# Kernel tuning notes

Hardware: AMD Instinct MI355X
Metric: run time of the kernel (lower is better)

The kernel has to match this reference:

```python
import jax, jax.numpy as jnp
import numpy as np

D = 1024
H = 16
HD = D // H  # 64


def setup_inputs() -> dict:
    key = jax.random.key(0)
    ks = jax.random.split(key, 12)
    B, S = 2, 2048
    inp = {
        "input_query": jax.random.normal(ks[0], (B, S, D), jnp.float32),
        "input_key": jax.random.normal(ks[1], (B, S, D), jnp.float32),
        "input_value": jax.random.normal(ks[2], (B, S, D), jnp.float32),
        "mask": jnp.ones((S, S), dtype=bool),  # ignored, as in original
        # per-head Q/K/V linears, stacked over heads: [H, D, HD]
        "Wq": jax.random.normal(ks[3], (H, D, HD), jnp.float32) / np.sqrt(D),
        "bq": jax.random.normal(ks[4], (H, HD), jnp.float32) * 0.01,
        "Wk": jax.random.normal(ks[5], (H, D, HD), jnp.float32) / np.sqrt(D),
        "bk": jax.random.normal(ks[6], (H, HD), jnp.float32) * 0.01,
        "Wv": jax.random.normal(ks[7], (H, D, HD), jnp.float32) / np.sqrt(D),
        "bv": jax.random.normal(ks[8], (H, HD), jnp.float32) * 0.01,
        "Wo": jax.random.normal(ks[9], (D, D), jnp.float32) / np.sqrt(D),
        "bo": jax.random.normal(ks[10], (D,), jnp.float32) * 0.01,
    }
    return inp


def reference(input_query, input_key, input_value, mask, Wq, bq, Wk, bk, Wv, bv, Wo, bo):
    B, S, _ = input_query.shape
    # batched per-head projections: [B,S,D] x [H,D,HD] -> [B,H,S,HD]
    q = jnp.einsum("bsd,hdk->bhsk", input_query, Wq) + bq[None, :, None, :]
    k = jnp.einsum("bsd,hdk->bhsk", input_key, Wk) + bk[None, :, None, :]
    v = jnp.einsum("bsd,hdk->bhsk", input_value, Wv) + bv[None, :, None, :]
    scale = 1.0 / np.sqrt(HD)
    scores = jnp.einsum("bhqk,bhsk->bhqs", q, k) * scale  # [B,H,S,S]
    causal = jnp.tril(jnp.ones((S, S), dtype=bool))
    scores = jnp.where(causal[None, None], scores, jnp.finfo(scores.dtype).min)
    p = jax.nn.softmax(scores, axis=-1)
    out = jnp.einsum("bhqs,bhsk->bhqk", p, v)  # [B,H,S,HD]
    # concat heads (matches torch.cat over head outputs on last dim)
    out = out.transpose(0, 2, 1, 3).reshape(B, S, D)
    return out @ Wo + bo
```

## Files before the change

kernel.cpp:

```cpp
#include <hip/hip_runtime.h>
#include <hip/hip_bf16.h>

typedef __bf16 bf16;
typedef bf16 bf16x8 __attribute__((ext_vector_type(8)));
typedef bf16 bf16x4 __attribute__((ext_vector_type(4)));
typedef float f32x4 __attribute__((ext_vector_type(4)));

#define B_  2
#define S_  2048
#define D_  1024
#define H_  16
#define HD_ 64
#define M_  4096
#define K_  1024
#define N_  1024

#if __has_builtin(__builtin_amdgcn_exp2f)
#define EXP2F(x) __builtin_amdgcn_exp2f(x)
#else
#define EXP2F(x) exp2f(x)
#endif

__device__ __forceinline__ void gld16(const bf16* g, bf16* l) {
    __builtin_amdgcn_global_load_lds(
        (const __attribute__((address_space(1))) unsigned int*)(g),
        (__attribute__((address_space(3))) unsigned int*)(l), 16, 0, 0);
}
__device__ __forceinline__ void gld16f(const float* g, float* l) {
    __builtin_amdgcn_global_load_lds(
        (const __attribute__((address_space(1))) unsigned int*)(g),
        (__attribute__((address_space(3))) unsigned int*)(l), 16, 0, 0);
}

__global__ void pack_w(const float* __restrict__ wq, const float* __restrict__ wk,
                       const float* __restrict__ wv, const float* __restrict__ wo,
                       bf16* __restrict__ out) {
    int t = blockIdx.y;
    bf16* dst = out + (size_t)t * N_ * K_;
    int o = blockIdx.x * 256 + threadIdx.x;
    int n = o >> 10, k = o & 1023;
    if (t == 3) {
        dst[o] = (bf16)wo[k * D_ + n];
    } else {
        const float* src = (t == 0) ? wq : (t == 1) ? wk : wv;
        dst[o] = (bf16)src[(n >> 6) * (D_ * HD_) + k * HD_ + (n & 63)];
    }
}

__global__ __launch_bounds__(256) void gemm_qkv(
        const float* __restrict__ xq, const float* __restrict__ xk,
        const float* __restrict__ xv, const bf16* __restrict__ Wt,
        const float* __restrict__ bq, const float* __restrict__ bk,
        const float* __restrict__ bv, bf16* __restrict__ QKV) {
    __shared__ __align__(16) float Af[2][128 * 32];
    __shared__ __align__(16) bf16 Bs[2][128 * 32];
    int t = blockIdx.z;
    const float* A = (t == 0) ? xq : (t == 1) ? xk : xv;
    const bf16* W = Wt + (size_t)t * N_ * K_;
    const float* bias = (t == 0) ? bq : (t == 1) ? bk : bv;
    int m0 = blockIdx.x * 128, n0 = blockIdx.y * 128;
    int tid = threadIdx.x;
    int w = tid >> 6, l = tid & 63, lr = l & 15, lg = l >> 4;
    int wr = (w >> 1) * 64, wc = (w & 1) * 64;
    int srow = (l >> 2), scol = (l & 3) * 8;
    size_t aoff[4];
    #pragma unroll
    for (int c = 0; c < 4; c++) {
        int chunk = w * 256 + c * 64 + l;
        int r = chunk >> 3, p = chunk & 7;
        aoff[c] = (size_t)(m0 + r) * K_ + ((p ^ (r & 7)) << 2);
    }
    f32x4 acc[4][4] = {};
    #pragma unroll
    for (int c = 0; c < 4; c++)
        gld16f(A + aoff[c], &Af[0][(w * 256 + c * 64) * 4]);
    #pragma unroll
    for (int c = 0; c < 2; c++) {
        int chunk = w * 2 + c;
        gld16(&W[(size_t)(n0 + chunk * 16 + srow) * K_ + scol], &Bs[0][chunk * 512]);
    }
    __syncthreads();
    for (int k0 = 0; k0 < K_; k0 += 32) {
        int cur = (k0 >> 5) & 1, nxt = cur ^ 1;
        if (k0 + 32 < K_) {
            #pragma unroll
            for (int c = 0; c < 4; c++)
                gld16f(A + aoff[c] + k0 + 32, &Af[nxt][(w * 256 + c * 64) * 4]);
            #pragma unroll
            for (int c = 0; c < 2; c++) {
                int chunk = w * 2 + c;
                gld16(&W[(size_t)(n0 + chunk * 16 + srow) * K_ + k0 + 32 + scol], &Bs[nxt][chunk * 512]);
            }
        }
        bf16x8 af[4], bfr[4];
        #pragma unroll
        for (int mi = 0; mi < 4; mi++) {
            int r = wr + mi * 16 + lr;
            f32x4 a0 = *(const f32x4*)((const char*)Af[cur] + r * 128 + (((lg * 2) ^ (r & 7)) * 16));
            f32x4 a1 = *(const f32x4*)((const char*)Af[cur] + r * 128 + (((lg * 2 + 1) ^ (r & 7)) * 16));
            bf16x8 v = { (bf16)a0[0], (bf16)a0[1], (bf16)a0[2], (bf16)a0[3],
                         (bf16)a1[0], (bf16)a1[1], (bf16)a1[2], (bf16)a1[3] };
            af[mi] = v;
        }
        #pragma unroll
        for (int ni = 0; ni < 4; ni++) bfr[ni] = *(const bf16x8*)&Bs[cur][(wc + ni * 16 + lr) * 32 + lg * 8];
        #pragma unroll
        for (int mi = 0; mi < 4; mi++)
            #pragma unroll
            for (int ni = 0; ni < 4; ni++)
                acc[mi][ni] = __builtin_amdgcn_mfma_f32_16x16x32_bf16(af[mi], bfr[ni], acc[mi][ni], 0, 0, 0);
        __syncthreads();
    }
    float qscale = (t == 0) ? 0.125f * 1.4426950408889634f : 1.0f;
    #pragma unroll
    for (int mi = 0; mi < 4; mi++)
        #pragma unroll
        for (int ni = 0; ni < 4; ni++)
            #pragma unroll
            for (int i = 0; i < 4; i++) {
                int m = m0 + wr + mi * 16 + lg * 4 + i;
                int n = n0 + wc + ni * 16 + lr;
                float v = (acc[mi][ni][i] + bias[n]) * qscale;
                int b = m >> 11, s = m & 2047, h = n >> 6, hd = n & 63;
                QKV[((((size_t)t * B_ + b) * H_ + h) * S_ + s) * HD_ + hd] = (bf16)v;
            }
}

__global__ __launch_bounds__(256) void gemm_out(
        const bf16* __restrict__ A, const bf16* __restrict__ Wt,
        const float* __restrict__ bo, float* __restrict__ out) {
    __shared__ __align__(16) bf16 As[2][128 * 32];
    __shared__ __align__(16) bf16 Bs[2][128 * 32];
    int m0 = blockIdx.x * 128, n0 = blockIdx.y * 128;
    int tid = threadIdx.x;
    int w = tid >> 6, l = tid & 63, lr = l & 15, lg = l >> 4;
    int wr = (w >> 1) * 64, wc = (w & 1) * 64;
    int srow = (l >> 2), scol = (l & 3) * 8;
    f32x4 acc[4][4] = {};
    #pragma unroll
    for (int c = 0; c < 2; c++) {
        int chunk = w * 2 + c;
        gld16(&A[(size_t)(m0 + chunk * 16 + srow) * K_ + scol], &As[0][chunk * 512]);
        gld16(&Wt[(size_t)(n0 + chunk * 16 + srow) * K_ + scol], &Bs[0][chunk * 512]);
    }
    __syncthreads();
    for (int k0 = 0; k0 < K_; k0 += 32) {
        int cur = (k0 >> 5) & 1, nxt = cur ^ 1;
        if (k0 + 32 < K_) {
            #pragma unroll
            for (int c = 0; c < 2; c++) {
                int chunk = w * 2 + c;
                gld16(&A[(size_t)(m0 + chunk * 16 + srow) * K_ + k0 + 32 + scol], &As[nxt][chunk * 512]);
                gld16(&Wt[(size_t)(n0 + chunk * 16 + srow) * K_ + k0 + 32 + scol], &Bs[nxt][chunk * 512]);
            }
        }
        bf16x8 af[4], bfr[4];
        #pragma unroll
        for (int mi = 0; mi < 4; mi++) af[mi] = *(const bf16x8*)&As[cur][(wr + mi * 16 + lr) * 32 + lg * 8];
        #pragma unroll
        for (int ni = 0; ni < 4; ni++) bfr[ni] = *(const bf16x8*)&Bs[cur][(wc + ni * 16 + lr) * 32 + lg * 8];
        #pragma unroll
        for (int mi = 0; mi < 4; mi++)
            #pragma unroll
            for (int ni = 0; ni < 4; ni++)
                acc[mi][ni] = __builtin_amdgcn_mfma_f32_16x16x32_bf16(af[mi], bfr[ni], acc[mi][ni], 0, 0, 0);
        __syncthreads();
    }
    #pragma unroll
    for (int mi = 0; mi < 4; mi++)
        #pragma unroll
        for (int ni = 0; ni < 4; ni++)
            #pragma unroll
            for (int i = 0; i < 4; i++) {
                int m = m0 + wr + mi * 16 + lg * 4 + i;
                int n = n0 + wc + ni * 16 + lr;
                out[(size_t)m * N_ + n] = acc[mi][ni][i] + bo[n];
            }
}

__global__ __launch_bounds__(256) void transpose_v(const bf16* __restrict__ V,
                                                   bf16* __restrict__ VT) {
    __shared__ __align__(16) bf16 Ls[64][64];
    int s0 = blockIdx.x * 64, bh = blockIdx.y;
    const bf16* src = V + (size_t)bh * S_ * HD_;
    bf16* dst = VT + (size_t)bh * HD_ * S_;
    int tid = threadIdx.x;
    #pragma unroll
    for (int c = tid; c < 512; c += 256) {
        int row = c >> 3, cg = (c & 7) * 8;
        int cgp = cg ^ (((row >> 3) & 3) << 4);
        *(bf16x8*)&Ls[row][cgp] = *(const bf16x8*)&src[(size_t)(s0 + row) * 64 + cg];
    }
    __syncthreads();
    #pragma unroll
    for (int c = tid; c < 512; c += 256) {
        int hd = c >> 3, sg = (c & 7) * 8;
        bf16x8 v;
        #pragma unroll
        for (int e = 0; e < 8; e++) {
            int row = sg + e;
            v[e] = Ls[row][hd ^ (((row >> 3) & 3) << 4)];
        }
        *(bf16x8*)&dst[(size_t)hd * S_ + s0 + sg] = v;
    }
}

__global__ __launch_bounds__(512) void attn(const bf16* __restrict__ QKV,
                                            const bf16* __restrict__ VT,
                                            bf16* __restrict__ AO) {
    __shared__ __align__(16) bf16 Ks[2][64][72];
    __shared__ __align__(16) bf16 Vts[2][64][72];
    __shared__ __align__(16) bf16 Ps[8][16][72];
    int bh = blockIdx.y;
    int qt = (bh & 16) ? blockIdx.x : (15 - blockIdx.x);
    int q0 = qt * 128;
    const bf16* Qp = QKV + (size_t)bh * S_ * HD_;
    const bf16* Kp = QKV + (size_t)(32 + bh) * S_ * HD_;
    const bf16* VTp = VT + (size_t)bh * HD_ * S_;
    int tid = threadIdx.x, w = tid >> 6, l = tid & 63, lr = l & 15, lg = l >> 4;
    int srow = tid >> 3, scg = (tid & 7) * 8;

    bf16x8 aq[2];
    #pragma unroll
    for (int ks = 0; ks < 2; ks++)
        aq[ks] = *(const bf16x8*)&Qp[(size_t)(q0 + w * 16 + lr) * 64 + ks * 32 + lg * 8];

    f32x4 o[4] = {};
    float lsum[4] = {};
    int jmax = 2 * qt + 1;

    *(bf16x8*)&Ks[0][srow][scg]  = *(const bf16x8*)&Kp[(size_t)srow * 64 + scg];
    *(bf16x8*)&Vts[0][srow][scg] = *(const bf16x8*)&VTp[(size_t)srow * S_ + scg];
    __syncthreads();

    for (int j = 0; j <= jmax; ++j) {
        int cur = j & 1;
        bool pf = (j < jmax);
        bf16x8 kreg, vreg;
        if (pf) {
            kreg = *(const bf16x8*)&Kp[(size_t)((j + 1) * 64 + srow) * 64 + scg];
            vreg = *(const bf16x8*)&VTp[(size_t)srow * S_ + (j + 1) * 64 + scg];
        }

        f32x4 sc[4] = {};
        __builtin_amdgcn_s_setprio(1);
        #pragma unroll
        for (int ks = 0; ks < 2; ks++)
            #pragma unroll
            for (int ni = 0; ni < 4; ni++) {
                bf16x8 bk_ = *(const bf16x8*)&Ks[cur][ni * 16 + lr][ks * 32 + lg * 8];
                sc[ni] = __builtin_amdgcn_mfma_f32_16x16x32_bf16(aq[ks], bk_, sc[ni], 0, 0, 0);
            }
        __builtin_amdgcn_s_setprio(0);

        int qrow = w * 16 + lg * 4;
        int kvb = j * 64 - q0;
        if (j >= 2 * qt) {
            #pragma unroll
            for (int ni = 0; ni < 4; ni++)
                #pragma unroll
                for (int i = 0; i < 4; i++) {
                    float s = sc[ni][i];
                    if (kvb + ni * 16 + lr > qrow + i) s = -30000.0f;
                    float p = EXP2F(s);
                    lsum[i] += p;
                    Ps[w][lg * 4 + i][ni * 16 + lr] = (bf16)p;
                }
        } else {
            #pragma unroll
            for (int ni = 0; ni < 4; ni++)
                #pragma unroll
                for (int i = 0; i < 4; i++) {
                    float p = EXP2F(sc[ni][i]);
                    lsum[i] += p;
                    Ps[w][lg * 4 + i][ni * 16 + lr] = (bf16)p;
                }
        }

        __builtin_amdgcn_s_setprio(1);
        #pragma unroll
        for (int ks = 0; ks < 2; ks++) {
            bf16x8 ap = *(const bf16x8*)&Ps[w][lr][ks * 32 + lg * 8];
            #pragma unroll
            for (int nf = 0; nf < 4; nf++) {
                bf16x8 bv_ = *(const bf16x8*)&Vts[cur][nf * 16 + lr][ks * 32 + lg * 8];
                o[nf] = __builtin_amdgcn_mfma_f32_16x16x32_bf16(ap, bv_, o[nf], 0, 0, 0);
            }
        }
        __builtin_amdgcn_s_setprio(0);

        if (pf) {
            *(bf16x8*)&Ks[cur ^ 1][srow][scg]  = kreg;
            *(bf16x8*)&Vts[cur ^ 1][srow][scg] = vreg;
        }
        __syncthreads();
    }

    #pragma unroll
    for (int i = 0; i < 4; i++) {
        #pragma unroll
        for (int xm = 1; xm < 16; xm <<= 1) lsum[i] += __shfl_xor(lsum[i], xm);
    }

    int b = bh >> 4, h = bh & 15;
    #pragma unroll
    for (int i = 0; i < 4; i++) {
        float inv = 1.0f / lsum[i];
        #pragma unroll
        for (int nf = 0; nf < 4; nf++) {
            int m = b * S_ + q0 + w * 16 + lg * 4 + i;
            int d = h * 64 + nf * 16 + lr;
            AO[(size_t)m * D_ + d] = (bf16)(o[nf][i] * inv);
        }
    }
}

extern "C" void kernel_launch(void* const* d_in, const int* in_sizes, int n_in,
                              void* d_out, int out_size, void* d_ws, size_t ws_size,
                              hipStream_t stream) {
    const float* xq = (const float*)d_in[0];
    const float* xk = (const float*)d_in[1];
    const float* xv = (const float*)d_in[2];
    const float* wq = (const float*)d_in[4];
    const float* bq = (const float*)d_in[5];
    const float* wk = (const float*)d_in[6];
    const float* bk = (const float*)d_in[7];
    const float* wv = (const float*)d_in[8];
    const float* bv = (const float*)d_in[9];
    const float* wo = (const float*)d_in[10];
    const float* bo = (const float*)d_in[11];
    float* out = (float*)d_out;

    bf16* Xb  = (bf16*)d_ws;
    bf16* Wb  = Xb  + (size_t)3 * M_ * K_;
    bf16* WoT = Wb  + (size_t)3 * N_ * K_;
    bf16* QKV = WoT + (size_t)N_ * K_;
    bf16* AO  = QKV + (size_t)3 * M_ * K_;
    bf16* VT  = Xb;

    pack_w <<<dim3(N_ * K_ / 256, 4), 256, 0, stream>>>(wq, wk, wv, wo, Wb);
    gemm_qkv<<<dim3(M_ / 128, N_ / 128, 3), 256, 0, stream>>>(xq, xk, xv, Wb, bq, bk, bv, QKV);
    transpose_v<<<dim3(S_ / 64, B_ * H_), 256, 0, stream>>>(QKV + (size_t)2 * M_ * K_, VT);
    attn    <<<dim3(S_ / 128, B_ * H_), 512, 0, stream>>>(QKV, VT, AO);
    gemm_out<<<dim3(M_ / 128, N_ / 128), 256, 0, stream>>>(AO, WoT, bo, out);
}
```

Baseline: 127.0 us.

## Transpose attention MFMA operands so each lane owns one query row

Swaps the A/B operands of both MFMAs so the accumulator layout puts one query row per lane and four consecutive key/dim columns in registers. Probabilities are then stored to a new packed LDS layout as 8-byte vectors instead of scalar bf16 writes. The row-sum reduction shrinks to two cross-lane shuffles, and output writes become 8-byte vectors. The aim is to cut LDS store count, shuffle work and scattered global stores, at the cost of a less padded P buffer that may see bank conflicts.

```diff
diff --git a/kernel.cpp b/kernel.cpp
--- a/kernel.cpp
+++ b/kernel.cpp
@@ -210,7 +210,7 @@
                                             bf16* __restrict__ AO) {
     __shared__ __align__(16) bf16 Ks[2][64][72];
     __shared__ __align__(16) bf16 Vts[2][64][72];
-    __shared__ __align__(16) bf16 Ps[8][16][72];
+    __shared__ __align__(16) bf16 Ps2[8][16][16][4];
     int bh = blockIdx.y;
     int qt = (bh & 16) ? blockIdx.x : (15 - blockIdx.x);
     int q0 = qt * 128;
@@ -226,7 +226,7 @@
         aq[ks] = *(const bf16x8*)&Qp[(size_t)(q0 + w * 16 + lr) * 64 + ks * 32 + lg * 8];
 
     f32x4 o[4] = {};
-    float lsum[4] = {};
+    float lsum = 0.0f;
     int jmax = 2 * qt + 1;
 
     *(bf16x8*)&Ks[0][srow][scg]  = *(const bf16x8*)&Kp[(size_t)srow * 64 + scg];
@@ -249,42 +249,51 @@
             #pragma unroll
             for (int ni = 0; ni < 4; ni++) {
                 bf16x8 bk_ = *(const bf16x8*)&Ks[cur][ni * 16 + lr][ks * 32 + lg * 8];
-                sc[ni] = __builtin_amdgcn_mfma_f32_16x16x32_bf16(aq[ks], bk_, sc[ni], 0, 0, 0);
+                sc[ni] = __builtin_amdgcn_mfma_f32_16x16x32_bf16(bk_, aq[ks], sc[ni], 0, 0, 0);
             }
         __builtin_amdgcn_s_setprio(0);
 
-        int qrow = w * 16 + lg * 4;
         int kvb = j * 64 - q0;
         if (j >= 2 * qt) {
             #pragma unroll
-            for (int ni = 0; ni < 4; ni++)
+            for (int ni = 0; ni < 4; ni++) {
+                float pv[4];
                 #pragma unroll
                 for (int i = 0; i < 4; i++) {
                     float s = sc[ni][i];
-                    if (kvb + ni * 16 + lr > qrow + i) s = -30000.0f;
+                    if (kvb + ni * 16 + lg * 4 + i > w * 16 + lr) s = -30000.0f;
                     float p = EXP2F(s);
-                    lsum[i] += p;
-                    Ps[w][lg * 4 + i][ni * 16 + lr] = (bf16)p;
+                    lsum += p;
+                    pv[i] = p;
                 }
+                bf16x4 pk = { (bf16)pv[0], (bf16)pv[1], (bf16)pv[2], (bf16)pv[3] };
+                *(bf16x4*)&Ps2[w][ni * 4 + lg][lr][0] = pk;
+            }
         } else {
             #pragma unroll
-            for (int ni = 0; ni < 4; ni++)
+            for (int ni = 0; ni < 4; ni++) {
+                float pv[4];
                 #pragma unroll
                 for (int i = 0; i < 4; i++) {
                     float p = EXP2F(sc[ni][i]);
-                    lsum[i] += p;
-                    Ps[w][lg * 4 + i][ni * 16 + lr] = (bf16)p;
+                    lsum += p;
+                    pv[i] = p;
                 }
+                bf16x4 pk = { (bf16)pv[0], (bf16)pv[1], (bf16)pv[2], (bf16)pv[3] };
+                *(bf16x4*)&Ps2[w][ni * 4 + lg][lr][0] = pk;
+            }
         }
 
         __builtin_amdgcn_s_setprio(1);
         #pragma unroll
         for (int ks = 0; ks < 2; ks++) {
-            bf16x8 ap = *(const bf16x8*)&Ps[w][lr][ks * 32 + lg * 8];
+            bf16x4 lo = *(const bf16x4*)&Ps2[w][8 * ks + 2 * lg + 0][lr][0];
+            bf16x4 hi = *(const bf16x4*)&Ps2[w][8 * ks + 2 * lg + 1][lr][0];
+            bf16x8 bq = __builtin_shufflevector(lo, hi, 0, 1, 2, 3, 4, 5, 6, 7);
             #pragma unroll
             for (int nf = 0; nf < 4; nf++) {
                 bf16x8 bv_ = *(const bf16x8*)&Vts[cur][nf * 16 + lr][ks * 32 + lg * 8];
-                o[nf] = __builtin_amdgcn_mfma_f32_16x16x32_bf16(ap, bv_, o[nf], 0, 0, 0);
+                o[nf] = __builtin_amdgcn_mfma_f32_16x16x32_bf16(bv_, bq, o[nf], 0, 0, 0);
             }
         }
         __builtin_amdgcn_s_setprio(0);
@@ -296,22 +305,17 @@
         __syncthreads();
     }
 
-    #pragma unroll
-    for (int i = 0; i < 4; i++) {
-        #pragma unroll
-        for (int xm = 1; xm < 16; xm <<= 1) lsum[i] += __shfl_xor(lsum[i], xm);
-    }
+    lsum += __shfl_xor(lsum, 16);
+    lsum += __shfl_xor(lsum, 32);
+    float inv = 1.0f / lsum;
 
     int b = bh >> 4, h = bh & 15;
-    #pragma unroll
-    for (int i = 0; i < 4; i++) {
-        float inv = 1.0f / lsum[i];
-        #pragma unroll
-        for (int nf = 0; nf < 4; nf++) {
-            int m = b * S_ + q0 + w * 16 + lg * 4 + i;
-            int d = h * 64 + nf * 16 + lr;
-            AO[(size_t)m * D_ + d] = (bf16)(o[nf][i] * inv);
-        }
+    int m = b * S_ + q0 + w * 16 + lr;
+    #pragma unroll
+    for (int nf = 0; nf < 4; nf++) {
+        bf16x4 ov = { (bf16)(o[nf][0] * inv), (bf16)(o[nf][1] * inv),
+                      (bf16)(o[nf][2] * inv), (bf16)(o[nf][3] * inv) };
+        *(bf16x4*)&AO[(size_t)m * D_ + h * 64 + nf * 16 + lg * 4] = ov;
     }
 }
 
```

After: 127.0 us. Within noise of the previous version (+0.0%).
